# Kernel optimization log

Measured on AMD Instinct MI355X. Metric: run time of the kernel, lower is better.

The kernel has to match this reference:

```python
import jax, jax.numpy as jnp
import numpy as np

N, E = 100000, 1600000
F_IN, HID, C, L = 512, 128, 64, 64
ALPHA, THETA = 0.1, 0.5


def setup_inputs() -> dict:
    key = jax.random.key(0)
    ks = jax.random.split(key, 6)
    x = jax.random.normal(ks[0], (N, F_IN), jnp.float32)
    edge_index = jax.random.randint(ks[1], (2, E), 0, N, jnp.int32)
    W_in = jax.random.normal(ks[2], (F_IN, HID), jnp.float32) * (1.0 / np.sqrt(F_IN))
    b_in = jnp.zeros((HID,), jnp.float32)
    W_convs = jax.random.normal(ks[3], (L, HID, HID), jnp.float32) * (1.0 / np.sqrt(HID))
    W_out = jax.random.normal(ks[4], (HID, C), jnp.float32) * (1.0 / np.sqrt(HID))
    b_out = jnp.zeros((C,), jnp.float32)
    return {"x": x, "edge_index": edge_index, "W_in": W_in, "b_in": b_in,
            "W_convs": W_convs, "W_out": W_out, "b_out": b_out}


def reference(x, edge_index, W_in, b_in, W_convs, W_out, b_out):
    src, dst = edge_index[0], edge_index[1]
    # gcn_norm with self loops: A_hat = D^-1/2 (A + I) D^-1/2
    deg = jax.ops.segment_sum(jnp.ones((E,), x.dtype), dst, num_segments=N) + 1.0
    dinv = jax.lax.rsqrt(deg)
    ew = dinv[src] * dinv[dst]          # [E] off-diagonal weights
    self_w = dinv * dinv                # [N] self-loop weights

    def spmm(h):  # h: [N, HID]
        agg = jax.ops.segment_sum(h[src] * ew[:, None], dst, num_segments=N)
        return agg + self_w[:, None] * h

    # beta_l = log(theta / l + 1), l = 1..L
    betas = jnp.log(THETA / jnp.arange(1, L + 1, dtype=x.dtype) + 1.0)

    x0 = jax.nn.relu(x @ W_in + b_in)   # [N, HID]

    def layer(h, lw):
        W, beta = lw
        p = spmm(h)
        t = (1.0 - ALPHA) * p + ALPHA * x0          # initial residual
        out = (1.0 - beta) * t + beta * (t @ W)     # identity mapping (shared weights)
        return jax.nn.relu(out), None

    z, _ = jax.lax.scan(layer, x0, (W_convs, betas))
    logits = z @ W_out + b_out
    return z, jax.nn.log_softmax(logits, axis=-1)
```

## Files before the change

### kernel.cpp

```cpp
#include <hip/hip_runtime.h>
#include <hip/hip_bf16.h>

#define NN 100000
#define NE 1600000
#define F_IN 512
#define HID 128
#define C_OUT 64
#define L_LAYERS 64
#define SCAN_NB 98

using short8 = __attribute__((ext_vector_type(8))) short;
using f32x4  = __attribute__((ext_vector_type(4))) float;
typedef __attribute__((ext_vector_type(4))) unsigned short ushort4v;

__device__ __forceinline__ short f2bf(float f) {
    __hip_bfloat16 h = __float2bfloat16(f);
    return __builtin_bit_cast(short, h);
}
__device__ __forceinline__ unsigned short f2bfu(float f) {
    __hip_bfloat16 h = __float2bfloat16(f);
    return __builtin_bit_cast(unsigned short, h);
}
__device__ __forceinline__ float bflo(unsigned u) { return __uint_as_float(u << 16); }
__device__ __forceinline__ float bfhi(unsigned u) { return __uint_as_float(u & 0xffff0000u); }
__device__ __forceinline__ float bf2f(unsigned short u) { return __uint_as_float((unsigned)u << 16); }


__global__ void count_deg(const int* __restrict__ dst, int* __restrict__ cnt) {
    int e = blockIdx.x * blockDim.x + threadIdx.x;
    if (e < NE) atomicAdd(&cnt[dst[e]], 1);
}

__global__ void compute_dinv(const int* __restrict__ cnt, float* __restrict__ dinv) {
    int n = blockIdx.x * blockDim.x + threadIdx.x;
    if (n < NN) dinv[n] = rsqrtf((float)cnt[n] + 1.0f);
}

__global__ __launch_bounds__(256) void scan1(const int* __restrict__ cnt,
                                             int* __restrict__ row_ptr,
                                             int* __restrict__ partial) {
    __shared__ int sdata[256];
    int tid = threadIdx.x;
    int base = blockIdx.x * 1024;
    int v[4];
    int idx0 = base + tid * 4;
#pragma unroll
    for (int i = 0; i < 4; ++i) {
        int idx = idx0 + i;
        v[i] = (idx < NN) ? cnt[idx] : 0;
    }
    int s = v[0] + v[1] + v[2] + v[3];
    sdata[tid] = s;
    __syncthreads();
    int x = s;
    for (int off = 1; off < 256; off <<= 1) {
        int y = (tid >= off) ? sdata[tid - off] : 0;
        __syncthreads();
        x += y;
        sdata[tid] = x;
        __syncthreads();
    }
    int run = x - s;
#pragma unroll
    for (int i = 0; i < 4; ++i) {
        int idx = idx0 + i;
        if (idx < NN) row_ptr[idx] = run;
        run += v[i];
    }
    if (tid == 255) partial[blockIdx.x] = x;
}

__global__ __launch_bounds__(128) void scan2(int* __restrict__ partial) {
    __shared__ int sdata[128];
    int tid = threadIdx.x;
    int v = (tid < SCAN_NB) ? partial[tid] : 0;
    sdata[tid] = v;
    __syncthreads();
    int x = v;
    for (int off = 1; off < 128; off <<= 1) {
        int y = (tid >= off) ? sdata[tid - off] : 0;
        __syncthreads();
        x += y;
        sdata[tid] = x;
        __syncthreads();
    }
    if (tid < SCAN_NB) partial[tid] = x - v;
}

__global__ void scan3(int* __restrict__ row_ptr, const int* __restrict__ partial) {
    int idx = blockIdx.x * blockDim.x + threadIdx.x;
    if (idx < NN) row_ptr[idx] += partial[idx >> 10];
    else if (idx <= NN + 64) row_ptr[idx] = NE;
}

__global__ void scatter_csr(const int* __restrict__ src, const int* __restrict__ dst,
                            const float* __restrict__ dinv, int* __restrict__ fill,
                            int2* __restrict__ edges) {
    int e = blockIdx.x * blockDim.x + threadIdx.x;
    if (e >= NE) return;
    int s = src[e], d = dst[e];
    int pos = atomicAdd(&fill[d], 1);
    edges[pos] = make_int2(s, __float_as_int(dinv[s] * dinv[d]));
}

__global__ __launch_bounds__(256) void prep_wt(const float* __restrict__ Wc,
                                               const float* __restrict__ Win,
                                               __hip_bfloat16* __restrict__ WT,
                                               __hip_bfloat16* __restrict__ WinT) {
    int b = blockIdx.x, tid = threadIdx.x;
    if (b < 64) {
        const float* src = Wc + (size_t)b * HID * HID;
        __hip_bfloat16* dstp = WT + (size_t)b * HID * HID;
        for (int it = 0; it < 64; ++it) {
            int idx = it * 256 + tid;
            int n = idx >> 7, k = idx & 127;
            dstp[idx] = __float2bfloat16(src[k * HID + n]);
        }
    } else {
        int j = b - 64;
        for (int it = 0; it < 16; ++it) {
            int gid = j * 4096 + it * 256 + tid;
            int n = gid >> 9, k = gid & 511;
            WinT[gid] = __float2bfloat16(Win[k * HID + n]);
        }
    }
}

__global__ __launch_bounds__(256) void gemm_x0_mfma(const float* __restrict__ X,
                                                    const __hip_bfloat16* __restrict__ WinT,
                                                    const float* __restrict__ bias,
                                                    __hip_bfloat16* __restrict__ X0b) {
    __shared__ short SMEM[128 * 128];
    int tid = threadIdx.x;
    int w = tid >> 6, l = tid & 63, g = l >> 4, r = l & 15;
    int row0 = blockIdx.x * 128;
    f32x4 acc[2][8] = {};

    float4 sx0[2], sx1[2];
    uint4 sw[2];
    auto load_regs = [&](int kt) {
        int k0 = kt * 32;
#pragma unroll
        for (int i = 0; i < 2; ++i) {
            int id = i * 256 + tid;
            int rr = id >> 2, slot = id & 3;
            int grow = row0 + rr;
            sx0[i] = make_float4(0.f, 0.f, 0.f, 0.f); sx1[i] = sx0[i];
            if (grow < NN) {
                sx0[i] = *(const float4*)&X[(size_t)grow * F_IN + k0 + slot * 8];
                sx1[i] = *(const float4*)&X[(size_t)grow * F_IN + k0 + slot * 8 + 4];
            }
            sw[i] = *(const uint4*)&WinT[(size_t)rr * F_IN + k0 + slot * 8];
        }
    };

    load_regs(0);
    for (int kt = 0; kt < 16; ++kt) {
        short* Xs = SMEM + (kt & 1) * 4096;
        short* Wsh = SMEM + 8192 + (kt & 1) * 4096;
#pragma unroll
        for (int i = 0; i < 2; ++i) {
            int id = i * 256 + tid;
            int rr = id >> 2, slot = id & 3;
            short8 p;
            p[0] = f2bf(sx0[i].x); p[1] = f2bf(sx0[i].y); p[2] = f2bf(sx0[i].z); p[3] = f2bf(sx0[i].w);
            p[4] = f2bf(sx1[i].x); p[5] = f2bf(sx1[i].y); p[6] = f2bf(sx1[i].z); p[7] = f2bf(sx1[i].w);
            *(short8*)&Xs[rr * 32 + (slot ^ ((rr >> 1) & 3)) * 8] = p;
            *(uint4*)&Wsh[rr * 32 + (slot ^ ((rr >> 1) & 3)) * 8] = sw[i];
        }
        __syncthreads();
        if (kt < 15) load_regs(kt + 1);
        short8 a[2], bb[8];
#pragma unroll
        for (int m = 0; m < 2; ++m) {
            int row = w * 32 + m * 16 + r;
            a[m] = *(short8*)&Xs[row * 32 + (g ^ ((row >> 1) & 3)) * 8];
        }
#pragma unroll
        for (int n = 0; n < 8; ++n) {
            int row = n * 16 + r;
            bb[n] = *(short8*)&Wsh[row * 32 + (g ^ ((row >> 1) & 3)) * 8];
        }
#pragma unroll
        for (int m = 0; m < 2; ++m)
#pragma unroll
            for (int n = 0; n < 8; ++n)
                acc[m][n] = __builtin_amdgcn_mfma_f32_16x16x32_bf16(a[m], bb[n], acc[m][n], 0, 0, 0);
    }
    __syncthreads();
#pragma unroll
    for (int m = 0; m < 2; ++m) {
#pragma unroll
        for (int n = 0; n < 8; ++n) {
            int col = n * 16 + r;
            float bv = bias[col];
#pragma unroll
            for (int q = 0; q < 4; ++q) {
                int row = w * 32 + m * 16 + g * 4 + q;
                float v = fmaxf(acc[m][n][q] + bv, 0.f);
                SMEM[row * 128 + ((col >> 3) ^ (row & 15)) * 8 + (col & 7)] = f2bf(v);
            }
        }
    }
    __syncthreads();
#pragma unroll
    for (int i = 0; i < 8; ++i) {
        int id = i * 256 + tid;
        int rr = id >> 4, c8 = id & 15;
        int grow = row0 + rr;
        if (grow < NN)
            *(uint4*)&X0b[(size_t)grow * HID + c8 * 8] =
                *(uint4*)&SMEM[rr * 128 + ((c8 ^ (rr & 15)) * 8)];
    }
}

__global__ __launch_bounds__(512, 6) void layer_fused(const unsigned* __restrict__ H2,
                                                      const unsigned* __restrict__ X02,
                                                      const float* __restrict__ dinv,
                                                      const int* __restrict__ row_ptr,
                                                      const int2* __restrict__ edges,
                                                      const __hip_bfloat16* __restrict__ WTl,
                                                      float beta,
                                                      __hip_bfloat16* __restrict__ Hout,
                                                      float* __restrict__ Zf) {
    __shared__ short Ts[64 * 128];
    __shared__ short Ws[128 * 128];
    int tid = threadIdx.x;
    int w = tid >> 6, l = tid & 63, g = l >> 4, r = l & 15;
    int row0 = blockIdx.x * 64;

#pragma unroll
    for (int i = 0; i < 4; ++i) {
        int id = i * 512 + tid;
        int rr = id >> 4, slot = id & 15;
        uint4 wv = *(const uint4*)&WTl[(size_t)id * 8];
        *(uint4*)&Ws[rr * 128 + (slot ^ (rr & 15)) * 8] = wv;
    }

    unsigned* TsU = (unsigned*)Ts;
    int nb0 = row0 + w * 8;
    int ep[9];
#pragma unroll
    for (int k = 0; k < 9; ++k) ep[k] = __builtin_amdgcn_readfirstlane(row_ptr[nb0 + k]);

#pragma unroll
    for (int j = 0; j < 4; ++j) {
        int rrA = w * 8 + 2 * j, rrB = rrA + 1;
        int nA = row0 + rrA, nB = nA + 1;
        bool vA = nA < NN, vB = nB < NN;
        unsigned hsA = vA ? H2[((unsigned)nA << 6) + l] : 0u;
        unsigned hsB = vB ? H2[((unsigned)nB << 6) + l] : 0u;
        unsigned xvA = vA ? X02[((unsigned)nA << 6) + l] : 0u;
        unsigned xvB = vB ? X02[((unsigned)nB << 6) + l] : 0u;
        float dvA = vA ? dinv[nA] : 0.f, dvB = vB ? dinv[nB] : 0.f;
        float a0A = dvA * dvA * bflo(hsA), a1A = dvA * dvA * bfhi(hsA);
        float a0B = dvB * dvB * bflo(hsB), a1B = dvB * dvB * bfhi(hsB);
        int eA = ep[2 * j], e1A = ep[2 * j + 1];
        int eB = e1A, e1B = ep[2 * j + 2];
        while (eA < e1A || eB < e1B) {
            int cA = e1A - eA; cA = cA > 8 ? 8 : (cA < 0 ? 0 : cA);
            int cB = e1B - eB; cB = cB > 8 ? 8 : (cB < 0 ? 0 : cB);
            int sA[8], sB[8];
            float wA[8], wB[8];
#pragma unroll
            for (int u = 0; u < 8; ++u) {
                int2 t = edges[eA + u];
                sA[u] = (u < cA) ? t.x : 0;
                wA[u] = (u < cA) ? __int_as_float(t.y) : 0.f;
            }
#pragma unroll
            for (int u = 0; u < 8; ++u) {
                int2 t = edges[eB + u];
                sB[u] = (u < cB) ? t.x : 0;
                wB[u] = (u < cB) ? __int_as_float(t.y) : 0.f;
            }
            unsigned hvA[8], hvB[8];
#pragma unroll
            for (int u = 0; u < 8; ++u) hvA[u] = H2[((unsigned)sA[u] << 6) + l];
#pragma unroll
            for (int u = 0; u < 8; ++u) hvB[u] = H2[((unsigned)sB[u] << 6) + l];
#pragma unroll
            for (int u = 0; u < 8; ++u) {
                a0A = fmaf(wA[u], bflo(hvA[u]), a0A);
                a1A = fmaf(wA[u], bfhi(hvA[u]), a1A);
                a0B = fmaf(wB[u], bflo(hvB[u]), a0B);
                a1B = fmaf(wB[u], bfhi(hvB[u]), a1B);
            }
            eA += cA; eB += cB;
        }
        a0A = 0.9f * a0A + 0.1f * bflo(xvA);  a1A = 0.9f * a1A + 0.1f * bfhi(xvA);
        a0B = 0.9f * a0B + 0.1f * bflo(xvB);  a1B = 0.9f * a1B + 0.1f * bfhi(xvB);
        unsigned pkA = (unsigned)f2bfu(a0A) | ((unsigned)f2bfu(a1A) << 16);
        unsigned pkB = (unsigned)f2bfu(a0B) | ((unsigned)f2bfu(a1B) << 16);
        TsU[rrA * 64 + ((l >> 2) ^ (rrA & 15)) * 4 + (l & 3)] = pkA;
        TsU[rrB * 64 + ((l >> 2) ^ (rrB & 15)) * 4 + (l & 3)] = pkB;
    }
    __syncthreads();

    int nb = w & 3, cg = w >> 2;
    f32x4 acc[4] = {};
#pragma unroll
    for (int ks = 0; ks < 4; ++ks) {
        int rrT = nb * 16 + r;
        short8 bT = *(short8*)&Ts[rrT * 128 + ((ks * 4 + g) ^ (rrT & 15)) * 8];
        short8 aW[4];
#pragma unroll
        for (int c = 0; c < 4; ++c) {
            int rrW = (cg * 4 + c) * 16 + r;
            aW[c] = *(short8*)&Ws[rrW * 128 + ((ks * 4 + g) ^ (rrW & 15)) * 8];
        }
#pragma unroll
        for (int c = 0; c < 4; ++c)
            acc[c] = __builtin_amdgcn_mfma_f32_16x16x32_bf16(aW[c], bT, acc[c], 0, 0, 0);
    }

    float omb = 1.0f - beta;
    int node = nb * 16 + r;
    int grow = row0 + node;
    if (grow < NN) {
#pragma unroll
        for (int c = 0; c < 4; ++c) {
            int c0 = (cg * 4 + c) * 16 + g * 4;
            int slotE = c0 >> 3, posE = c0 & 7;
            ushort4v tv = *(ushort4v*)&Ts[node * 128 + (slotE ^ (node & 15)) * 8 + posE];
            float o[4];
#pragma unroll
            for (int q = 0; q < 4; ++q)
                o[q] = fmaxf(omb * bf2f(tv[q]) + beta * acc[c][q], 0.f);
            if (Zf) {
                *(float4*)&Zf[(size_t)grow * HID + c0] = make_float4(o[0], o[1], o[2], o[3]);
            } else {
                ushort4v hv;
#pragma unroll
                for (int q = 0; q < 4; ++q) hv[q] = f2bfu(o[q]);
                *(ushort4v*)&Hout[(size_t)grow * HID + c0] = hv;
            }
        }
    }
}

__global__ __launch_bounds__(64) void final_kernel(const float* __restrict__ Z,
                                                   const float* __restrict__ Wout,
                                                   const float* __restrict__ bout,
                                                   float* __restrict__ lo) {
    int n = blockIdx.x;
    int c = threadIdx.x;
    float logit = bout[c];
    for (int k = 0; k < HID; ++k) {
        logit = fmaf(Z[(size_t)n * HID + k], Wout[k * C_OUT + c], logit);
    }
    float m = logit;
#pragma unroll
    for (int off = 32; off; off >>= 1) m = fmaxf(m, __shfl_xor(m, off));
    float ex = __expf(logit - m);
    float ssum = ex;
#pragma unroll
    for (int off = 32; off; off >>= 1) ssum += __shfl_xor(ssum, off);
    lo[(size_t)n * C_OUT + c] = logit - m - logf(ssum);
}

extern "C" void kernel_launch(void* const* d_in, const int* in_sizes, int n_in,
                              void* d_out, int out_size, void* d_ws, size_t ws_size,
                              hipStream_t stream) {
    const float* x = (const float*)d_in[0];
    const int* ei = (const int*)d_in[1];
    const int* src = ei;
    const int* dst = ei + NE;
    const float* W_in = (const float*)d_in[2];
    const float* b_in = (const float*)d_in[3];
    const float* W_convs = (const float*)d_in[4];
    const float* W_out = (const float*)d_in[5];
    const float* b_out = (const float*)d_in[6];
    float* out = (float*)d_out;

    char* ws = (char*)d_ws;
    float* dinv = (float*)ws;              ws += (size_t)NN * 4;
    int* row_ptr = (int*)ws;               ws += (size_t)(NN + 72) * 4;
    int* fill = (int*)ws;                  ws += (size_t)NN * 4;
    int* partial = (int*)ws;               ws += (size_t)128 * 4;
    int2* edges = (int2*)ws;               ws += (size_t)(NE + 8) * 8;
    __hip_bfloat16* WT = (__hip_bfloat16*)ws;   ws += (size_t)L_LAYERS * HID * HID * 2;
    __hip_bfloat16* WinT = (__hip_bfloat16*)ws; ws += (size_t)F_IN * HID * 2;
    __hip_bfloat16* x0b = (__hip_bfloat16*)ws;  ws += (size_t)NN * HID * 2;
    __hip_bfloat16* HbA = (__hip_bfloat16*)ws;  ws += (size_t)NN * HID * 2;
    __hip_bfloat16* HbB = (__hip_bfloat16*)ws;  ws += (size_t)NN * HID * 2;

    hipMemsetAsync(fill, 0, (size_t)NN * 4, stream);
    count_deg<<<(NE + 255) / 256, 256, 0, stream>>>(dst, fill);
    compute_dinv<<<(NN + 255) / 256, 256, 0, stream>>>(fill, dinv);
    scan1<<<SCAN_NB, 256, 0, stream>>>(fill, row_ptr, partial);
    scan2<<<1, 128, 0, stream>>>(partial);
    scan3<<<(NN + 255) / 256, 256, 0, stream>>>(row_ptr, partial);
    hipMemcpyAsync(fill, row_ptr, (size_t)NN * 4, hipMemcpyDeviceToDevice, stream);
    scatter_csr<<<(NE + 255) / 256, 256, 0, stream>>>(src, dst, dinv, fill, edges);
    prep_wt<<<80, 256, 0, stream>>>(W_convs, W_in, WT, WinT);

    int gemm_blocks = (NN + 127) / 128;
    gemm_x0_mfma<<<gemm_blocks, 256, 0, stream>>>(x, WinT, b_in, x0b);

    int layer_blocks = (NN + 63) / 64;
    float* zf = out;
    for (int l = 0; l < L_LAYERS; ++l) {
        const __hip_bfloat16* h_in = (l == 0) ? x0b : ((l & 1) ? HbA : HbB);
        __hip_bfloat16* h_out = (l & 1) ? HbB : HbA;
        float beta = logf(0.5f / (float)(l + 1) + 1.0f);
        bool last = (l == L_LAYERS - 1);
        layer_fused<<<layer_blocks, 512, 0, stream>>>(
            (const unsigned*)h_in, (const unsigned*)x0b, dinv, row_ptr, edges,
            WT + (size_t)l * HID * HID, beta,
            h_out, last ? zf : (float*)nullptr);
    }

    final_kernel<<<NN, 64, 0, stream>>>(zf, W_out, b_out, out + (size_t)NN * HID);
}
```

Baseline: 6.369 ms.

## Split wavefront halves across node pairs, shrink layer blocks, read W from global

The per-layer fused SpMM+GEMM kernel now uses 256-thread blocks of 32 nodes. Each half-wave gathers one node's row with 8-byte loads, with 16 edges in flight per iteration instead of 8. The weight matrix is no longer staged in shared memory and MFMA operands are read directly from global/L2, cutting LDS use so more blocks fit per CU. The x0 GEMM prefetch also becomes two register sets deep. The trade-off is redundant edge loads per half-wave and repeated global weight reads across many more blocks.

```diff
diff --git a/kernel.cpp b/kernel.cpp
--- a/kernel.cpp
+++ b/kernel.cpp
@@ -126,6 +126,59 @@
     }
 }
 
+#define LOAD_SET(X0V, X1V, WVV, KT)                                              \
+    {                                                                            \
+        int k0_ = (KT) * 32;                                                     \
+        _Pragma("unroll")                                                        \
+        for (int i = 0; i < 2; ++i) {                                            \
+            int id = i * 256 + tid;                                              \
+            int rr = id >> 2, slot = id & 3;                                     \
+            int grow = row0 + rr;                                                \
+            X0V[i] = make_float4(0.f, 0.f, 0.f, 0.f); X1V[i] = X0V[i];           \
+            if (grow < NN) {                                                     \
+                X0V[i] = *(const float4*)&X[(size_t)grow * F_IN + k0_ + slot * 8];     \
+                X1V[i] = *(const float4*)&X[(size_t)grow * F_IN + k0_ + slot * 8 + 4]; \
+            }                                                                    \
+            WVV[i] = *(const uint4*)&WinT[(size_t)rr * F_IN + k0_ + slot * 8];   \
+        }                                                                        \
+    }
+
+#define PHASE(X0V, X1V, WVV, KT, BUF)                                            \
+    {                                                                            \
+        short* Xs = SMEM + (BUF) * 4096;                                         \
+        short* Wsh = SMEM + 8192 + (BUF) * 4096;                                 \
+        _Pragma("unroll")                                                        \
+        for (int i = 0; i < 2; ++i) {                                            \
+            int id = i * 256 + tid;                                              \
+            int rr = id >> 2, slot = id & 3;                                     \
+            short8 p;                                                            \
+            p[0] = f2bf(X0V[i].x); p[1] = f2bf(X0V[i].y);                        \
+            p[2] = f2bf(X0V[i].z); p[3] = f2bf(X0V[i].w);                        \
+            p[4] = f2bf(X1V[i].x); p[5] = f2bf(X1V[i].y);                        \
+            p[6] = f2bf(X1V[i].z); p[7] = f2bf(X1V[i].w);                        \
+            *(short8*)&Xs[rr * 32 + (slot ^ ((rr >> 1) & 3)) * 8] = p;           \
+            *(uint4*)&Wsh[rr * 32 + (slot ^ ((rr >> 1) & 3)) * 8] = WVV[i];      \
+        }                                                                        \
+        __syncthreads();                                                         \
+        if ((KT) < 14) LOAD_SET(X0V, X1V, WVV, (KT) + 2);                        \
+        short8 a[2], bb[8];                                                      \
+        _Pragma("unroll")                                                        \
+        for (int m = 0; m < 2; ++m) {                                            \
+            int row = w * 32 + m * 16 + r;                                       \
+            a[m] = *(short8*)&Xs[row * 32 + (g ^ ((row >> 1) & 3)) * 8];         \
+        }                                                                        \
+        _Pragma("unroll")                                                        \
+        for (int n = 0; n < 8; ++n) {                                            \
+            int row = n * 16 + r;                                                \
+            bb[n] = *(short8*)&Wsh[row * 32 + (g ^ ((row >> 1) & 3)) * 8];       \
+        }                                                                        \
+        _Pragma("unroll")                                                        \
+        for (int m = 0; m < 2; ++m)                                              \
+            _Pragma("unroll")                                                    \
+            for (int n = 0; n < 8; ++n)                                          \
+                acc[m][n] = __builtin_amdgcn_mfma_f32_16x16x32_bf16(a[m], bb[n], acc[m][n], 0, 0, 0); \
+    }
+
 __global__ __launch_bounds__(256) void gemm_x0_mfma(const float* __restrict__ X,
                                                     const __hip_bfloat16* __restrict__ WinT,
                                                     const float* __restrict__ bias,
@@ -136,56 +189,14 @@
     int row0 = blockIdx.x * 128;
     f32x4 acc[2][8] = {};
 
-    float4 sx0[2], sx1[2];
-    uint4 sw[2];
-    auto load_regs = [&](int kt) {
-        int k0 = kt * 32;
-#pragma unroll
-        for (int i = 0; i < 2; ++i) {
-            int id = i * 256 + tid;
-            int rr = id >> 2, slot = id & 3;
-            int grow = row0 + rr;
-            sx0[i] = make_float4(0.f, 0.f, 0.f, 0.f); sx1[i] = sx0[i];
-            if (grow < NN) {
-                sx0[i] = *(const float4*)&X[(size_t)grow * F_IN + k0 + slot * 8];
-                sx1[i] = *(const float4*)&X[(size_t)grow * F_IN + k0 + slot * 8 + 4];
-            }
-            sw[i] = *(const uint4*)&WinT[(size_t)rr * F_IN + k0 + slot * 8];
-        }
-    };
-
-    load_regs(0);
-    for (int kt = 0; kt < 16; ++kt) {
-        short* Xs = SMEM + (kt & 1) * 4096;
-        short* Wsh = SMEM + 8192 + (kt & 1) * 4096;
-#pragma unroll
-        for (int i = 0; i < 2; ++i) {
-            int id = i * 256 + tid;
-            int rr = id >> 2, slot = id & 3;
-            short8 p;
-            p[0] = f2bf(sx0[i].x); p[1] = f2bf(sx0[i].y); p[2] = f2bf(sx0[i].z); p[3] = f2bf(sx0[i].w);
-            p[4] = f2bf(sx1[i].x); p[5] = f2bf(sx1[i].y); p[6] = f2bf(sx1[i].z); p[7] = f2bf(sx1[i].w);
-            *(short8*)&Xs[rr * 32 + (slot ^ ((rr >> 1) & 3)) * 8] = p;
-            *(uint4*)&Wsh[rr * 32 + (slot ^ ((rr >> 1) & 3)) * 8] = sw[i];
-        }
-        __syncthreads();
-        if (kt < 15) load_regs(kt + 1);
-        short8 a[2], bb[8];
-#pragma unroll
-        for (int m = 0; m < 2; ++m) {
-            int row = w * 32 + m * 16 + r;
-            a[m] = *(short8*)&Xs[row * 32 + (g ^ ((row >> 1) & 3)) * 8];
-        }
-#pragma unroll
-        for (int n = 0; n < 8; ++n) {
-            int row = n * 16 + r;
-            bb[n] = *(short8*)&Wsh[row * 32 + (g ^ ((row >> 1) & 3)) * 8];
-        }
-#pragma unroll
-        for (int m = 0; m < 2; ++m)
-#pragma unroll
-            for (int n = 0; n < 8; ++n)
-                acc[m][n] = __builtin_amdgcn_mfma_f32_16x16x32_bf16(a[m], bb[n], acc[m][n], 0, 0, 0);
+    float4 ax0[2], ax1[2]; uint4 aw[2];
+    float4 bx0[2], bx1[2]; uint4 bw[2];
+
+    LOAD_SET(ax0, ax1, aw, 0);
+    LOAD_SET(bx0, bx1, bw, 1);
+    for (int kt = 0; kt < 16; kt += 2) {
+        PHASE(ax0, ax1, aw, kt, 0);
+        PHASE(bx0, bx1, bw, kt + 1, 1);
     }
     __syncthreads();
 #pragma unroll
@@ -214,8 +225,8 @@
     }
 }
 
-__global__ __launch_bounds__(512, 6) void layer_fused(const unsigned* __restrict__ H2,
-                                                      const unsigned* __restrict__ X02,
+__global__ __launch_bounds__(256, 4) void layer_fused(const uint2* __restrict__ H8,
+                                                      const uint2* __restrict__ X08,
                                                       const float* __restrict__ dinv,
                                                       const int* __restrict__ row_ptr,
                                                       const int2* __restrict__ edges,
@@ -223,21 +234,14 @@
                                                       float beta,
                                                       __hip_bfloat16* __restrict__ Hout,
                                                       float* __restrict__ Zf) {
-    __shared__ short Ts[64 * 128];
-    __shared__ short Ws[128 * 128];
+    __shared__ short Ts[32 * 128];
     int tid = threadIdx.x;
     int w = tid >> 6, l = tid & 63, g = l >> 4, r = l & 15;
-    int row0 = blockIdx.x * 64;
-
-#pragma unroll
-    for (int i = 0; i < 4; ++i) {
-        int id = i * 512 + tid;
-        int rr = id >> 4, slot = id & 15;
-        uint4 wv = *(const uint4*)&WTl[(size_t)id * 8];
-        *(uint4*)&Ws[rr * 128 + (slot ^ (rr & 15)) * 8] = wv;
-    }
-
+    int h = l >> 5;
+    int q = l & 31;
+    int row0 = blockIdx.x * 32;
     unsigned* TsU = (unsigned*)Ts;
+
     int nb0 = row0 + w * 8;
     int ep[9];
 #pragma unroll
@@ -245,59 +249,55 @@
 
 #pragma unroll
     for (int j = 0; j < 4; ++j) {
-        int rrA = w * 8 + 2 * j, rrB = rrA + 1;
-        int nA = row0 + rrA, nB = nA + 1;
-        bool vA = nA < NN, vB = nB < NN;
-        unsigned hsA = vA ? H2[((unsigned)nA << 6) + l] : 0u;
-        unsigned hsB = vB ? H2[((unsigned)nB << 6) + l] : 0u;
-        unsigned xvA = vA ? X02[((unsigned)nA << 6) + l] : 0u;
-        unsigned xvB = vB ? X02[((unsigned)nB << 6) + l] : 0u;
-        float dvA = vA ? dinv[nA] : 0.f, dvB = vB ? dinv[nB] : 0.f;
-        float a0A = dvA * dvA * bflo(hsA), a1A = dvA * dvA * bfhi(hsA);
-        float a0B = dvB * dvB * bflo(hsB), a1B = dvB * dvB * bfhi(hsB);
+        int rrA = w * 8 + 2 * j;
+        int nA = row0 + rrA;
+        int myn = nA + h;
+        bool vmy = myn < NN;
+        uint2 hs = vmy ? H8[(size_t)(unsigned)myn * 32 + q] : make_uint2(0u, 0u);
+        uint2 xv = vmy ? X08[(size_t)(unsigned)myn * 32 + q] : make_uint2(0u, 0u);
+        float dv = vmy ? dinv[myn] : 0.f;
+        float sw = dv * dv;
+        float a0 = sw * bflo(hs.x), a1 = sw * bfhi(hs.x);
+        float a2 = sw * bflo(hs.y), a3 = sw * bfhi(hs.y);
         int eA = ep[2 * j], e1A = ep[2 * j + 1];
         int eB = e1A, e1B = ep[2 * j + 2];
         while (eA < e1A || eB < e1B) {
-            int cA = e1A - eA; cA = cA > 8 ? 8 : (cA < 0 ? 0 : cA);
-            int cB = e1B - eB; cB = cB > 8 ? 8 : (cB < 0 ? 0 : cB);
-            int sA[8], sB[8];
-            float wA[8], wB[8];
-#pragma unroll
-            for (int u = 0; u < 8; ++u) {
-                int2 t = edges[eA + u];
-                sA[u] = (u < cA) ? t.x : 0;
-                wA[u] = (u < cA) ? __int_as_float(t.y) : 0.f;
+            int cA = e1A - eA; cA = cA > 16 ? 16 : (cA < 0 ? 0 : cA);
+            int cB = e1B - eB; cB = cB > 16 ? 16 : (cB < 0 ? 0 : cB);
+            uint2 hv[16];
+            float ww[16];
+#pragma unroll
+            for (int u = 0; u < 16; ++u) {
+                int2 tA = edges[eA + u];
+                int2 tB = edges[eB + u];
+                int sA = (u < cA) ? tA.x : 0;
+                float wAu = (u < cA) ? __int_as_float(tA.y) : 0.f;
+                int sB = (u < cB) ? tB.x : 0;
+                float wBu = (u < cB) ? __int_as_float(tB.y) : 0.f;
+                int s = h ? sB : sA;
+                ww[u] = h ? wBu : wAu;
+                hv[u] = H8[(size_t)(unsigned)s * 32 + q];
             }
 #pragma unroll
-            for (int u = 0; u < 8; ++u) {
-                int2 t = edges[eB + u];
-                sB[u] = (u < cB) ? t.x : 0;
-                wB[u] = (u < cB) ? __int_as_float(t.y) : 0.f;
-            }
-            unsigned hvA[8], hvB[8];
-#pragma unroll
-            for (int u = 0; u < 8; ++u) hvA[u] = H2[((unsigned)sA[u] << 6) + l];
-#pragma unroll
-            for (int u = 0; u < 8; ++u) hvB[u] = H2[((unsigned)sB[u] << 6) + l];
-#pragma unroll
-            for (int u = 0; u < 8; ++u) {
-                a0A = fmaf(wA[u], bflo(hvA[u]), a0A);
-                a1A = fmaf(wA[u], bfhi(hvA[u]), a1A);
-                a0B = fmaf(wB[u], bflo(hvB[u]), a0B);
-                a1B = fmaf(wB[u], bfhi(hvB[u]), a1B);
+            for (int u = 0; u < 16; ++u) {
+                a0 = fmaf(ww[u], bflo(hv[u].x), a0);
+                a1 = fmaf(ww[u], bfhi(hv[u].x), a1);
+                a2 = fmaf(ww[u], bflo(hv[u].y), a2);
+                a3 = fmaf(ww[u], bfhi(hv[u].y), a3);
             }
             eA += cA; eB += cB;
         }
-        a0A = 0.9f * a0A + 0.1f * bflo(xvA);  a1A = 0.9f * a1A + 0.1f * bfhi(xvA);
-        a0B = 0.9f * a0B + 0.1f * bflo(xvB);  a1B = 0.9f * a1B + 0.1f * bfhi(xvB);
-        unsigned pkA = (unsigned)f2bfu(a0A) | ((unsigned)f2bfu(a1A) << 16);
-        unsigned pkB = (unsigned)f2bfu(a0B) | ((unsigned)f2bfu(a1B) << 16);
-        TsU[rrA * 64 + ((l >> 2) ^ (rrA & 15)) * 4 + (l & 3)] = pkA;
-        TsU[rrB * 64 + ((l >> 2) ^ (rrB & 15)) * 4 + (l & 3)] = pkB;
+        a0 = 0.9f * a0 + 0.1f * bflo(xv.x);  a1 = 0.9f * a1 + 0.1f * bfhi(xv.x);
+        a2 = 0.9f * a2 + 0.1f * bflo(xv.y);  a3 = 0.9f * a3 + 0.1f * bfhi(xv.y);
+        unsigned pk0 = (unsigned)f2bfu(a0) | ((unsigned)f2bfu(a1) << 16);
+        unsigned pk1 = (unsigned)f2bfu(a2) | ((unsigned)f2bfu(a3) << 16);
+        int rr = rrA + h;
+        *(uint2*)&TsU[rr * 64 + (((q >> 1) ^ (rr & 15)) << 2) + (q & 1) * 2] =
+            make_uint2(pk0, pk1);
     }
     __syncthreads();
 
-    int nb = w & 3, cg = w >> 2;
+    int nb = w & 1, cg = w >> 1;
     f32x4 acc[4] = {};
 #pragma unroll
     for (int ks = 0; ks < 4; ++ks) {
@@ -306,8 +306,8 @@
         short8 aW[4];
 #pragma unroll
         for (int c = 0; c < 4; ++c) {
-            int rrW = (cg * 4 + c) * 16 + r;
-            aW[c] = *(short8*)&Ws[rrW * 128 + ((ks * 4 + g) ^ (rrW & 15)) * 8];
+            int rowW = (cg * 4 + c) * 16 + r;
+            aW[c] = *(const short8*)&WTl[(size_t)rowW * 128 + (ks * 4 + g) * 8];
         }
 #pragma unroll
         for (int c = 0; c < 4; ++c)
@@ -325,14 +325,14 @@
             ushort4v tv = *(ushort4v*)&Ts[node * 128 + (slotE ^ (node & 15)) * 8 + posE];
             float o[4];
 #pragma unroll
-            for (int q = 0; q < 4; ++q)
-                o[q] = fmaxf(omb * bf2f(tv[q]) + beta * acc[c][q], 0.f);
+            for (int p = 0; p < 4; ++p)
+                o[p] = fmaxf(omb * bf2f(tv[p]) + beta * acc[c][p], 0.f);
             if (Zf) {
                 *(float4*)&Zf[(size_t)grow * HID + c0] = make_float4(o[0], o[1], o[2], o[3]);
             } else {
                 ushort4v hv;
 #pragma unroll
-                for (int q = 0; q < 4; ++q) hv[q] = f2bfu(o[q]);
+                for (int p = 0; p < 4; ++p) hv[p] = f2bfu(o[p]);
                 *(ushort4v*)&Hout[(size_t)grow * HID + c0] = hv;
             }
         }
@@ -378,7 +378,7 @@
     int* row_ptr = (int*)ws;               ws += (size_t)(NN + 72) * 4;
     int* fill = (int*)ws;                  ws += (size_t)NN * 4;
     int* partial = (int*)ws;               ws += (size_t)128 * 4;
-    int2* edges = (int2*)ws;               ws += (size_t)(NE + 8) * 8;
+    int2* edges = (int2*)ws;               ws += (size_t)(NE + 16) * 8;
     __hip_bfloat16* WT = (__hip_bfloat16*)ws;   ws += (size_t)L_LAYERS * HID * HID * 2;
     __hip_bfloat16* WinT = (__hip_bfloat16*)ws; ws += (size_t)F_IN * HID * 2;
     __hip_bfloat16* x0b = (__hip_bfloat16*)ws;  ws += (size_t)NN * HID * 2;
@@ -398,15 +398,15 @@
     int gemm_blocks = (NN + 127) / 128;
     gemm_x0_mfma<<<gemm_blocks, 256, 0, stream>>>(x, WinT, b_in, x0b);
 
-    int layer_blocks = (NN + 63) / 64;
+    int layer_blocks = (NN + 31) / 32;
     float* zf = out;
     for (int l = 0; l < L_LAYERS; ++l) {
         const __hip_bfloat16* h_in = (l == 0) ? x0b : ((l & 1) ? HbA : HbB);
         __hip_bfloat16* h_out = (l & 1) ? HbB : HbA;
         float beta = logf(0.5f / (float)(l + 1) + 1.0f);
         bool last = (l == L_LAYERS - 1);
-        layer_fused<<<layer_blocks, 512, 0, stream>>>(
-            (const unsigned*)h_in, (const unsigned*)x0b, dinv, row_ptr, edges,
+        layer_fused<<<layer_blocks, 256, 0, stream>>>(
+            (const uint2*)h_in, (const uint2*)x0b, dinv, row_ptr, edges,
             WT + (size_t)l * HID * HID, beta,
             h_out, last ? zf : (float*)nullptr);
     }
```

Result: slower. 7.117 ms (+11.8%).
